# Performance work log

Hardware: AMD Instinct MI355X
Metric: run time of the kernel (lower is better)

The kernel has to match this reference:

```python
import jax, jax.numpy as jnp
import numpy as np
from jax import lax

B, T, D, U, M = 64, 800, 3, 400, 20


def _lstm_peephole(x, Wx, Wh, b, p_i, p_f, p_o):
    """Peephole LSTM over [B,T,Din] -> [B,T,U]. Gate order: i,f,c,o."""
    xW = jnp.einsum('btd,dg->btg', x, Wx) + b  # precompute input projection [B,T,4U]
    h0 = jnp.zeros((x.shape[0], U), x.dtype)
    c0 = jnp.zeros((x.shape[0], U), x.dtype)

    def step(carry, xt):
        h, c = carry
        z = xt + h @ Wh
        zi, zf, zc, zo = jnp.split(z, 4, axis=-1)
        i = jax.nn.sigmoid(zi + p_i * c)
        f = jax.nn.sigmoid(zf + p_f * c)
        c_new = f * c + i * jnp.tanh(zc)
        o = jax.nn.sigmoid(zo + p_o * c_new)
        h_new = o * jnp.tanh(c_new)
        return (h_new, c_new), h_new

    _, hs = lax.scan(step, (h0, c0), jnp.swapaxes(xW, 0, 1))  # [T,B,U]
    return jnp.swapaxes(hs, 0, 1)


def _mdn(h, Wmdn, bmdn):
    y = h @ Wmdn + bmdn  # [B,T,6M+1]
    pi = jax.nn.softmax(y[..., :M], axis=-1)
    mu1 = y[..., M:2 * M]
    mu2 = y[..., 2 * M:3 * M]
    s1 = jnp.exp(y[..., 3 * M:4 * M])
    s2 = jnp.exp(y[..., 4 * M:5 * M])
    rho = jnp.tanh(y[..., 5 * M:6 * M])
    eos = jax.nn.sigmoid(y[..., 6 * M:])
    return jnp.concatenate([pi, mu1, mu2, s1, s2, rho, eos], axis=-1)


def setup_inputs() -> dict:
    key = jax.random.key(0)
    ks = jax.random.split(key, 32)
    s = 0.08
    inp = {'x': jax.random.normal(ks[0], (B, T, D), jnp.float32)}
    k = 1
    for l in range(3):
        din = D if l == 0 else D + U
        inp[f'Wx{l}'] = jax.random.normal(ks[k], (din, 4 * U), jnp.float32) * s; k += 1
        inp[f'Wh{l}'] = jax.random.normal(ks[k], (U, 4 * U), jnp.float32) * s; k += 1
        inp[f'b{l}'] = jnp.zeros((4 * U,), jnp.float32)
        inp[f'peep_i{l}'] = jax.random.normal(ks[k], (U,), jnp.float32) * s; k += 1
        inp[f'peep_f{l}'] = jax.random.normal(ks[k], (U,), jnp.float32) * s; k += 1
        inp[f'peep_o{l}'] = jax.random.normal(ks[k], (U,), jnp.float32) * s; k += 1
    inp['Wmdn'] = jax.random.normal(ks[k], (U, 6 * M + 1), jnp.float32) * s
    inp['bmdn'] = jnp.zeros((6 * M + 1,), jnp.float32)
    return inp


def reference(x, Wx0, Wh0, b0, peep_i0, peep_f0, peep_o0,
              Wx1, Wh1, b1, peep_i1, peep_f1, peep_o1,
              Wx2, Wh2, b2, peep_i2, peep_f2, peep_o2,
              Wmdn, bmdn):
    h = _lstm_peephole(x, Wx0, Wh0, b0, peep_i0, peep_f0, peep_o0)
    # skip connections: layers 1,2 take concat([inputs, prev_hidden])
    h = _lstm_peephole(jnp.concatenate([x, h], axis=-1), Wx1, Wh1, b1, peep_i1, peep_f1, peep_o1)
    h = _lstm_peephole(jnp.concatenate([x, h], axis=-1), Wx2, Wh2, b2, peep_i2, peep_f2, peep_o2)
    return _mdn(h, Wmdn, bmdn)
```

## Files before the change

kernel.cpp:

```cpp
#include <hip/hip_runtime.h>


#define TSTEPS 800
#define NG 4
#define GB 16
#define NSL 5
#define UB 80
#define CB 320
#define KP 416
#define RD 16
#define HXD 4
#define AS 424
#define ZS 332

typedef __attribute__((ext_vector_type(8))) __bf16 bf16x8;
typedef __attribute__((ext_vector_type(4))) float floatx4;

struct Peeps { const float* pi[3]; const float* pf[3]; const float* po[3]; };

__device__ __forceinline__ unsigned short f2bf(float f) {
    unsigned int u = __float_as_uint(f);
    return (unsigned short)((u + 0x7FFFu + ((u >> 16) & 1u)) >> 16);
}
__device__ __forceinline__ float bf_lo(unsigned u) { return __uint_as_float(u << 16); }
__device__ __forceinline__ float bf_hi(unsigned u) { return __uint_as_float(u & 0xFFFF0000u); }
__device__ __forceinline__ float sigm_(float v) { return 1.f / (1.f + __expf(-v)); }
__device__ __forceinline__ float tanh_(float v) { float e = __expf(2.f * v); return 1.f - 2.f / (e + 1.f); }
__device__ __forceinline__ unsigned ld_a(const unsigned* p) {
    return __hip_atomic_load(p, __ATOMIC_RELAXED, __HIP_MEMORY_SCOPE_AGENT);
}
__device__ __forceinline__ void st_a(unsigned* p, unsigned v) {
    __hip_atomic_store(p, v, __ATOMIC_RELAXED, __HIP_MEMORY_SCOPE_AGENT);
}

__global__ void pack_rec(const float* __restrict__ Wx, const float* __restrict__ Wh,
                         const float* __restrict__ bias, unsigned short* __restrict__ dst,
                         int is_l0) {
    int idx = blockIdx.x * 256 + threadIdx.x;
    if (idx >= 1600 * KP) return;
    int col = idx / KP, k = idx - col * KP;
    int co = (col & 3) * 400 + (col >> 2);
    float v = 0.f;
    if (k < 400) v = Wh[k * 1600 + co];
    else if (is_l0) {
        if (k < 403) v = Wx[(k - 400) * 1600 + co];
        else if (k == 403) v = bias[co];
    }
    dst[idx] = f2bf(v);
}
__global__ void pack_pre(const float* __restrict__ Wx, const float* __restrict__ bias,
                         unsigned short* __restrict__ dst) {
    int idx = blockIdx.x * 256 + threadIdx.x;
    if (idx >= 1600 * KP) return;
    int col = idx / KP, k = idx - col * KP;
    int co = (col & 3) * 400 + (col >> 2);
    float v = 0.f;
    if (k < 400) v = Wx[(3 + k) * 1600 + co];
    else if (k < 403) v = Wx[(k - 400) * 1600 + co];
    else if (k == 403) v = bias[co];
    dst[idx] = f2bf(v);
}
__global__ void pack_x(const float* __restrict__ x, unsigned short* __restrict__ xp) {
    int idx = blockIdx.x * 256 + threadIdx.x;
    if (idx >= TSTEPS * 64) return;
    int t = idx / 64, b = idx - t * 64;
    unsigned short o[4];
    for (int d = 0; d < 3; ++d) o[d] = f2bf(x[(b * TSTEPS + t) * 3 + d]);
    o[3] = 0x3F80u;
    *(uint2*)(xp + (size_t)idx * 4) = *(uint2*)o;
}
__global__ void pack_mdn(const float* __restrict__ Wm, const float* __restrict__ bm,
                         unsigned short* __restrict__ dst) {
    int idx = blockIdx.x * 256 + threadIdx.x;
    if (idx >= 128 * KP) return;
    int col = idx / KP, k = idx - col * KP;
    float v = 0.f;
    if (col < 121) {
        if (k < 400) v = Wm[k * 121 + col];
        else if (k == 400) v = bm[col];
    }
    dst[idx] = f2bf(v);
}

__global__ __launch_bounds__(640)
void fused_scan(const unsigned short* __restrict__ Bp,
                const unsigned short* __restrict__ Bpre,
                const unsigned short* __restrict__ xpack,
                unsigned* __restrict__ hx,
                unsigned* __restrict__ hring,
                unsigned* __restrict__ zin,
                unsigned* __restrict__ seqb,
                unsigned* __restrict__ h2,
                Peeps pp) {
    const int tid = threadIdx.x;
    const int lane = tid & 63;
    const int w = tid >> 6;
    const int bid = blockIdx.x;

    const int xcd = bid & 7;
    const int slot = bid >> 3;
    int g, rl = -1, rs = 0, plz = -1, psp = 0;
    if (xcd < 4) {
        g = xcd;
        if (slot < 5)       { rl = 0; rs = slot; }
        else if (slot < 10) { rl = 2; rs = slot - 5; }
        else                { plz = 1; psp = slot - 10; }
    } else {
        g = xcd - 4;
        if (slot < 5)       { rl = 1; rs = slot; }
        else if (slot < 10) { plz = 0; psp = slot - 5; }
        else return;
    }

    __shared__ unsigned short A[32 * AS];
    __shared__ float Z[16 * ZS];

    for (int i = tid; i < 32 * AS; i += 640) A[i] = 0;

    const int er = tid / 40;
    const int up = tid - er * 40;
    const int aoff = (lane & 15) * AS + ((lane >> 4) << 3);
    const int zc0 = w * 32 + (lane & 15);
    const int zr = (lane >> 4) << 2;

    if (rl >= 0) {
        const int l = rl;
        const int s = rs;
        bf16x8 breg[2][13];
        #pragma unroll
        for (int n = 0; n < 2; ++n) {
            const unsigned short* bpp = Bp + (size_t)l * 1600 * KP
                + (size_t)(s * CB + w * 32 + n * 16 + (lane & 15)) * KP + ((lane >> 4) << 3);
            #pragma unroll
            for (int kt = 0; kt < 13; ++kt) breg[n][kt] = *(const bf16x8*)(bpp + kt * 32);
        }
        unsigned* hxL = hx + (size_t)(l * NG + g) * HXD * 6400;
        unsigned* ringL = hring + (size_t)(l * NG + g) * RD * 3200;
        const unsigned* zinL = zin + (size_t)((l - 1) * NG + g) * RD * 12800;
        unsigned* FHown = seqb + ((l * NG + g) * NSL + s) * 16;
        const unsigned* FZup = seqb + (60 + ((l - 1) * NG + g) * NSL) * 16;
        const unsigned* FZdn = seqb + (60 + (l * NG + g) * NSL) * 16;

        const int p0 = ((s + 1) % 5) * 80, p1 = ((s + 2) % 5) * 80;
        const int p2 = ((s + 3) % 5) * 80, p3 = ((s + 4) % 5) * 80;
        const int ug0 = s * UB + 2 * up;
        const float pi0 = pp.pi[l][ug0], pi1 = pp.pi[l][ug0 + 1];
        const float pf0 = pp.pf[l][ug0], pf1 = pp.pf[l][ug0 + 1];
        const float po0 = pp.po[l][ug0], po1 = pp.po[l][ug0 + 1];
        float c0 = 0.f, c1 = 0.f;

        __syncthreads();
        if (l == 0 && tid < 16)
            *(uint2*)(&A[tid * AS + 400]) = *(const uint2*)(xpack + ((size_t)0 * 64 + g * 16 + tid) * 4);
        __syncthreads();

        for (int t = 0; t < TSTEPS; ++t) {
            {
                const unsigned want = (unsigned)(t - 1) << 16;
                const unsigned* hb = hxL + (size_t)((t + 3) & 3) * 6400 + er * 400 + 2 * up;
                const unsigned* fp = nullptr; unsigned fneed = 0;
                if (l > 0 && (t & 3) == 0 && tid < NSL) { fp = FZup + tid * 16; fneed = (unsigned)(t + 4); }
                else if (l < 2 && (t & 7) == 0 && tid >= NSL && tid < 2 * NSL) {
                    fp = FZdn + (tid - NSL) * 16; fneed = (unsigned)(t > 8 ? t - 8 : 0);
                }
                unsigned v0, v1, v2, v3, v4, v5, v6, v7;
                for (;;) {
                    bool ok = true;
                    if (t > 0) {
                        v0 = ld_a(hb + p0); v1 = ld_a(hb + p0 + 1);
                        v2 = ld_a(hb + p1); v3 = ld_a(hb + p1 + 1);
                        v4 = ld_a(hb + p2); v5 = ld_a(hb + p2 + 1);
                        v6 = ld_a(hb + p3); v7 = ld_a(hb + p3 + 1);
                        ok = ((v0 & 0xFFFF0000u) == want) & ((v1 & 0xFFFF0000u) == want) &
                             ((v2 & 0xFFFF0000u) == want) & ((v3 & 0xFFFF0000u) == want) &
                             ((v4 & 0xFFFF0000u) == want) & ((v5 & 0xFFFF0000u) == want) &
                             ((v6 & 0xFFFF0000u) == want) & ((v7 & 0xFFFF0000u) == want);
                    }
                    if (fp) ok &= (ld_a(fp) >= fneed);
                    if (__all(ok)) break;
                }
                if (t > 0) {
                    const int ab = er * AS + 2 * up;
                    *(unsigned*)&A[ab + p0] = (v0 & 0xFFFFu) | (v1 << 16);
                    *(unsigned*)&A[ab + p1] = (v2 & 0xFFFFu) | (v3 << 16);
                    *(unsigned*)&A[ab + p2] = (v4 & 0xFFFFu) | (v5 << 16);
                    *(unsigned*)&A[ab + p3] = (v6 & 0xFFFFu) | (v7 << 16);
                }
            }
            __syncthreads();
            if (tid == 0) st_a(FHown, (unsigned)t);

            unsigned q0, q1, q2, q3;
            if (l > 0) {
                const unsigned* zp = zinL + (size_t)(t & 15) * 12800 + er * 800 + 4 * (s * 40 + up);
                q0 = ld_a(zp); q1 = ld_a(zp + 1); q2 = ld_a(zp + 2); q3 = ld_a(zp + 3);
            }

            floatx4 a0 = {0, 0, 0, 0}, a1 = {0, 0, 0, 0};
            #pragma unroll
            for (int kt = 0; kt < 13; ++kt) {
                bf16x8 a = *(const bf16x8*)(&A[aoff + kt * 32]);
                a0 = __builtin_amdgcn_mfma_f32_16x16x32_bf16(a, breg[0][kt], a0, 0, 0, 0);
                a1 = __builtin_amdgcn_mfma_f32_16x16x32_bf16(a, breg[1][kt], a1, 0, 0, 0);
            }
            #pragma unroll
            for (int ri = 0; ri < 4; ++ri) {
                Z[(zr + ri) * ZS + zc0] = a0[ri];
                Z[(zr + ri) * ZS + zc0 + 16] = a1[ri];
            }
            __syncthreads();

            float4 za = *(const float4*)(&Z[er * ZS + 8 * up]);
            float4 zb4 = *(const float4*)(&Z[er * ZS + 8 * up + 4]);
            if (l > 0) {
                za.x += bf_lo(q0); za.y += bf_hi(q0); za.z += bf_lo(q1); za.w += bf_hi(q1);
                zb4.x += bf_lo(q2); zb4.y += bf_hi(q2); zb4.z += bf_lo(q3); zb4.w += bf_hi(q3);
            }
            float iv = sigm_(za.x + pi0 * c0);
            float fv = sigm_(za.y + pf0 * c0);
            float cn = fv * c0 + iv * tanh_(za.z);
            float ov = sigm_(za.w + po0 * cn);
            float h0 = ov * tanh_(cn);
            c0 = cn;
            iv = sigm_(zb4.x + pi1 * c1);
            fv = sigm_(zb4.y + pf1 * c1);
            cn = fv * c1 + iv * tanh_(zb4.z);
            ov = sigm_(zb4.w + po1 * cn);
            float h1 = ov * tanh_(cn);
            c1 = cn;
            unsigned packh = (unsigned)f2bf(h0) | ((unsigned)f2bf(h1) << 16);
            *(unsigned*)&A[er * AS + ug0] = packh;
            if (l == 0 && tid < 16 && t + 1 < TSTEPS)
                *(uint2*)(&A[tid * AS + 400]) = *(const uint2*)(xpack + ((size_t)(t + 1) * 64 + g * 16 + tid) * 4);
            __syncthreads();

            unsigned* hxs = hxL + (size_t)(t & 3) * 6400 + er * 400 + ug0;
            st_a(hxs, ((unsigned)t << 16) | (packh & 0xFFFFu));
            st_a(hxs + 1, ((unsigned)t << 16) | (packh >> 16));
            if (l < 2)
                st_a(ringL + (size_t)(t & 15) * 3200 + er * 200 + s * 40 + up, packh);
            else
                h2[(size_t)t * 12800 + (g * GB + er) * 200 + s * 40 + up] = packh;
        }
        __syncthreads();
        if (tid == 0) st_a(FHown, (unsigned)TSTEPS);
    } else {
        const int lz = plz;
        const int sp = psp;
        bf16x8 breg[2][13];
        #pragma unroll
        for (int n = 0; n < 2; ++n) {
            const unsigned short* bpp = Bpre + (size_t)lz * 1600 * KP
                + (size_t)(sp * CB + w * 32 + n * 16 + (lane & 15)) * KP + ((lane >> 4) << 3);
            #pragma unroll
            for (int kt = 0; kt < 13; ++kt) breg[n][kt] = *(const bf16x8*)(bpp + kt * 32);
        }
        const unsigned* ringS = hring + (size_t)(lz * NG + g) * RD * 3200;
        unsigned* zinD = zin + (size_t)(lz * NG + g) * RD * 12800;
        const unsigned* FHup = seqb + ((lz * NG + g) * NSL) * 16;
        const unsigned* FHdn = seqb + (((lz + 1) * NG + g) * NSL) * 16;
        unsigned* FZown = seqb + (60 + (lz * NG + g) * NSL + sp) * 16;
        __syncthreads();

        for (int c = 0; c < TSTEPS; c += 2) {
            {
                const unsigned* fp = nullptr; unsigned need = 0;
                if (tid < NSL) { fp = FHup + tid * 16; need = (unsigned)(c + 2); }
                else if (tid < 2 * NSL) { fp = FHdn + (tid - NSL) * 16; need = (unsigned)(c > 14 ? c - 14 : 0); }
                bool ok = (fp == nullptr) || (ld_a(fp) >= need);
                while (!__all(ok)) { if (!ok) ok = ld_a(fp) >= need; }
            }
            __syncthreads();
            if (tid == 0 && c > 0) st_a(FZown, (unsigned)c);

            for (int i = tid; i < 6400; i += 640) {
                int tc = (i >= 3200) ? 1 : 0;
                int j = i - tc * 3200;
                unsigned v = ld_a(ringS + (size_t)((c + tc) & 15) * 3200 + j);
                int r = j / 200, d = j - r * 200;
                *(unsigned*)&A[(tc * 16 + r) * AS + 2 * d] = v;
            }
            if (tid < 32) {
                int tc = tid >> 4, r = tid & 15;
                *(uint2*)(&A[(tc * 16 + r) * AS + 400]) =
                    *(const uint2*)(xpack + ((size_t)(c + tc) * 64 + g * 16 + r) * 4);
            }
            __syncthreads();

            floatx4 a00 = {0,0,0,0}, a01 = {0,0,0,0}, a10 = {0,0,0,0}, a11 = {0,0,0,0};
            #pragma unroll
            for (int kt = 0; kt < 13; ++kt) {
                bf16x8 x0 = *(const bf16x8*)(&A[aoff + kt * 32]);
                bf16x8 x1 = *(const bf16x8*)(&A[aoff + 16 * AS + kt * 32]);
                a00 = __builtin_amdgcn_mfma_f32_16x16x32_bf16(x0, breg[0][kt], a00, 0, 0, 0);
                a01 = __builtin_amdgcn_mfma_f32_16x16x32_bf16(x0, breg[1][kt], a01, 0, 0, 0);
                a10 = __builtin_amdgcn_mfma_f32_16x16x32_bf16(x1, breg[0][kt], a10, 0, 0, 0);
                a11 = __builtin_amdgcn_mfma_f32_16x16x32_bf16(x1, breg[1][kt], a11, 0, 0, 0);
            }
            #pragma unroll
            for (int m = 0; m < 2; ++m) {
                #pragma unroll
                for (int ri = 0; ri < 4; ++ri) {
                    Z[(zr + ri) * ZS + zc0] = (m ? a10[ri] : a00[ri]);
                    Z[(zr + ri) * ZS + zc0 + 16] = (m ? a11[ri] : a01[ri]);
                }
                __syncthreads();
                float4 za = *(const float4*)(&Z[er * ZS + 8 * up]);
                float4 zbv = *(const float4*)(&Z[er * ZS + 8 * up + 4]);
                unsigned* zg = zinD + (size_t)((c + m) & 15) * 12800 + er * 800 + sp * 160 + 4 * up;
                st_a(zg,     (unsigned)f2bf(za.x) | ((unsigned)f2bf(za.y) << 16));
                st_a(zg + 1, (unsigned)f2bf(za.z) | ((unsigned)f2bf(za.w) << 16));
                st_a(zg + 2, (unsigned)f2bf(zbv.x) | ((unsigned)f2bf(zbv.y) << 16));
                st_a(zg + 3, (unsigned)f2bf(zbv.z) | ((unsigned)f2bf(zbv.w) << 16));
                __syncthreads();
            }
        }
        __syncthreads();
        if (tid == 0) st_a(FZown, (unsigned)TSTEPS);
    }
}

__global__ __launch_bounds__(256)
void mdn_kernel(const unsigned short* __restrict__ h2,
                const unsigned short* __restrict__ Bm,
                float* __restrict__ out) {
    const int blk = blockIdx.x;
    const int b = blk / 25;
    const int t0 = (blk - b * 25) * 32;
    const int tid = threadIdx.x;
    const int lane = tid & 63;
    const int w = tid >> 6;
    const int m = w & 1, nh = w >> 1;

    __shared__ unsigned short A[32 * 424];
    __shared__ float Z[32 * 132];
    __shared__ float rmax[32], rinv[32];

    for (int i = tid; i < 32 * 424; i += 256) A[i] = 0;
    __syncthreads();
    for (int c = tid; c < 32 * 50; c += 256) {
        int r = c / 50, j = c - r * 50;
        *(bf16x8*)(&A[r * 424 + j * 8]) = *(const bf16x8*)(h2 + (size_t)(t0 + r) * 25600 + b * 400 + j * 8);
    }
    if (tid < 32) A[tid * 424 + 400] = 0x3F80u;
    __syncthreads();

    floatx4 acc[4] = {{0,0,0,0},{0,0,0,0},{0,0,0,0},{0,0,0,0}};
    const int aoff = (m * 16 + (lane & 15)) * 424 + ((lane >> 4) << 3);
    #pragma unroll
    for (int kt = 0; kt < 13; ++kt) {
        bf16x8 a = *(const bf16x8*)(&A[aoff + kt * 32]);
        #pragma unroll
        for (int n = 0; n < 4; ++n) {
            const unsigned short* bp = Bm + (size_t)((nh * 4 + n) * 16 + (lane & 15)) * KP
                                          + ((lane >> 4) << 3) + kt * 32;
            acc[n] = __builtin_amdgcn_mfma_f32_16x16x32_bf16(a, *(const bf16x8*)bp, acc[n], 0, 0, 0);
        }
    }
    #pragma unroll
    for (int n = 0; n < 4; ++n) {
        int zc = (nh * 4 + n) * 16 + (lane & 15);
        int zrow = m * 16 + ((lane >> 4) << 2);
        #pragma unroll
        for (int ri = 0; ri < 4; ++ri)
            Z[(zrow + ri) * 132 + zc] = acc[n][ri];
    }
    __syncthreads();
    if (tid < 32) {
        float mx = -1e30f;
        for (int j = 0; j < 20; ++j) mx = fmaxf(mx, Z[tid * 132 + j]);
        float sm = 0.f;
        for (int j = 0; j < 20; ++j) sm += __expf(Z[tid * 132 + j] - mx);
        rmax[tid] = mx;
        rinv[tid] = 1.f / sm;
    }
    __syncthreads();
    for (int idxo = tid; idxo < 32 * 121; idxo += 256) {
        int r = idxo / 121, jo = idxo - r * 121;
        float v = Z[r * 132 + jo];
        float o;
        if (jo < 20) o = __expf(v - rmax[r]) * rinv[r];
        else if (jo < 60) o = v;
        else if (jo < 100) o = __expf(v);
        else if (jo < 120) o = tanh_(v);
        else o = sigm_(v);
        out[(size_t)(b * TSTEPS + t0 + r) * 121 + jo] = o;
    }
}

extern "C" void kernel_launch(void* const* d_in, const int* in_sizes, int n_in,
                              void* d_out, int out_size, void* d_ws, size_t ws_size,
                              hipStream_t stream) {
    const float* x = (const float*)d_in[0];
    const float* Wx[3] = {(const float*)d_in[1], (const float*)d_in[7], (const float*)d_in[13]};
    const float* Wh[3] = {(const float*)d_in[2], (const float*)d_in[8], (const float*)d_in[14]};
    const float* bb[3] = {(const float*)d_in[3], (const float*)d_in[9], (const float*)d_in[15]};
    Peeps pp;
    for (int l = 0; l < 3; ++l) {
        pp.pi[l] = (const float*)d_in[4 + 6 * l];
        pp.pf[l] = (const float*)d_in[5 + 6 * l];
        pp.po[l] = (const float*)d_in[6 + 6 * l];
    }
    const float* Wm = (const float*)d_in[19];
    const float* bm = (const float*)d_in[20];
    float* out = (float*)d_out;

    char* base = (char*)d_ws;
    size_t off = 0;
    auto alloc = [&](size_t bytes) -> void* {
        void* r = base + off;
        off = (off + bytes + 255) & ~(size_t)255;
        return r;
    };
    unsigned* seqb        = (unsigned*)alloc(1600 * sizeof(unsigned));
    unsigned* hx          = (unsigned*)alloc((size_t)3 * NG * HXD * 6400 * 4);
    unsigned* hring       = (unsigned*)alloc((size_t)3 * NG * RD * 3200 * 4);
    unsigned* zin         = (unsigned*)alloc((size_t)2 * NG * RD * 12800 * 4);
    unsigned short* Bp    = (unsigned short*)alloc((size_t)3 * 1600 * KP * 2);
    unsigned short* Bpre  = (unsigned short*)alloc((size_t)2 * 1600 * KP * 2);
    unsigned short* Bm    = (unsigned short*)alloc((size_t)128 * KP * 2);
    unsigned short* xpk   = (unsigned short*)alloc((size_t)TSTEPS * 64 * 4 * 2);
    unsigned short* h2    = (unsigned short*)alloc((size_t)TSTEPS * 64 * 400 * 2);

    hipMemsetAsync(seqb, 0, 1600 * sizeof(unsigned), stream);
    hipMemsetAsync(hx, 0xAA, (size_t)3 * NG * HXD * 6400 * 4, stream);

    for (int l = 0; l < 3; ++l)
        pack_rec<<<2600, 256, 0, stream>>>(Wx[l], Wh[l], bb[l], Bp + (size_t)l * 1600 * KP, l == 0);
    pack_pre<<<2600, 256, 0, stream>>>(Wx[1], bb[1], Bpre);
    pack_pre<<<2600, 256, 0, stream>>>(Wx[2], bb[2], Bpre + (size_t)1600 * KP);
    pack_x<<<200, 256, 0, stream>>>(x, xpk);
    pack_mdn<<<208, 256, 0, stream>>>(Wm, bm, Bm);

    fused_scan<<<120, 640, 0, stream>>>(Bp, Bpre, xpk, hx, hring, zin, seqb,
                                        (unsigned*)h2, pp);

    mdn_kernel<<<1600, 256, 0, stream>>>(h2, Bm, out);
}
```

Before: 3.038 ms.

## Remap Z staging layout to avoid bank conflicts and drop barriers

Changes the LDS staging layout of MFMA gate results so each MFMA lane writes into a strided slot. The elementwise threads then read their 8 gate values with stride-40 scalar loads instead of float4 loads, aiming to cut LDS bank conflicts. The recurrent loop drops the barrier after the h write. The precompute path double-buffers Z so both timesteps are staged and read under one barrier instead of four. Removing barriers relies on later synchronisation to protect the A and Z buffers; if any hazard remains, the results can race.

```diff
diff --git a/kernel.cpp b/kernel.cpp
--- a/kernel.cpp
+++ b/kernel.cpp
@@ -113,15 +113,16 @@
     }
 
     __shared__ unsigned short A[32 * AS];
-    __shared__ float Z[16 * ZS];
+    __shared__ float Z[2 * 16 * ZS];
 
     for (int i = tid; i < 32 * AS; i += 640) A[i] = 0;
 
     const int er = tid / 40;
     const int up = tid - er * 40;
-    const int aoff = (lane & 15) * AS + ((lane >> 4) << 3);
-    const int zc0 = w * 32 + (lane & 15);
+    const int cc = lane & 15;
+    const int aoff = cc * AS + ((lane >> 4) << 3);
     const int zr = (lane >> 4) << 2;
+    const int slotA = (cc & 7) * 40 + w * 4 + (cc >> 3);
 
     if (rl >= 0) {
         const int l = rl;
@@ -130,7 +131,7 @@
         #pragma unroll
         for (int n = 0; n < 2; ++n) {
             const unsigned short* bpp = Bp + (size_t)l * 1600 * KP
-                + (size_t)(s * CB + w * 32 + n * 16 + (lane & 15)) * KP + ((lane >> 4) << 3);
+                + (size_t)(s * CB + w * 32 + n * 16 + cc) * KP + ((lane >> 4) << 3);
             #pragma unroll
             for (int kt = 0; kt < 13; ++kt) breg[n][kt] = *(const bf16x8*)(bpp + kt * 32);
         }
@@ -205,13 +206,17 @@
             }
             #pragma unroll
             for (int ri = 0; ri < 4; ++ri) {
-                Z[(zr + ri) * ZS + zc0] = a0[ri];
-                Z[(zr + ri) * ZS + zc0 + 16] = a1[ri];
+                Z[(zr + ri) * ZS + slotA] = a0[ri];
+                Z[(zr + ri) * ZS + slotA + 2] = a1[ri];
             }
             __syncthreads();
 
-            float4 za = *(const float4*)(&Z[er * ZS + 8 * up]);
-            float4 zb4 = *(const float4*)(&Z[er * ZS + 8 * up + 4]);
+            float zv[8];
+            #pragma unroll
+            for (int k = 0; k < 8; ++k)
+                zv[k] = Z[er * ZS + 40 * k + up];
+            float4 za = {zv[0], zv[1], zv[2], zv[3]};
+            float4 zb4 = {zv[4], zv[5], zv[6], zv[7]};
             if (l > 0) {
                 za.x += bf_lo(q0); za.y += bf_hi(q0); za.z += bf_lo(q1); za.w += bf_hi(q1);
                 zb4.x += bf_lo(q2); zb4.y += bf_hi(q2); zb4.z += bf_lo(q3); zb4.w += bf_hi(q3);
@@ -232,7 +237,6 @@
             *(unsigned*)&A[er * AS + ug0] = packh;
             if (l == 0 && tid < 16 && t + 1 < TSTEPS)
                 *(uint2*)(&A[tid * AS + 400]) = *(const uint2*)(xpack + ((size_t)(t + 1) * 64 + g * 16 + tid) * 4);
-            __syncthreads();
 
             unsigned* hxs = hxL + (size_t)(t & 3) * 6400 + er * 400 + ug0;
             st_a(hxs, ((unsigned)t << 16) | (packh & 0xFFFFu));
@@ -251,7 +255,7 @@
         #pragma unroll
         for (int n = 0; n < 2; ++n) {
             const unsigned short* bpp = Bpre + (size_t)lz * 1600 * KP
-                + (size_t)(sp * CB + w * 32 + n * 16 + (lane & 15)) * KP + ((lane >> 4) << 3);
+                + (size_t)(sp * CB + w * 32 + n * 16 + cc) * KP + ((lane >> 4) << 3);
             #pragma unroll
             for (int kt = 0; kt < 13; ++kt) breg[n][kt] = *(const bf16x8*)(bpp + kt * 32);
         }
@@ -298,22 +302,30 @@
                 a11 = __builtin_amdgcn_mfma_f32_16x16x32_bf16(x1, breg[1][kt], a11, 0, 0, 0);
             }
             #pragma unroll
-            for (int m = 0; m < 2; ++m) {
-                #pragma unroll
-                for (int ri = 0; ri < 4; ++ri) {
-                    Z[(zr + ri) * ZS + zc0] = (m ? a10[ri] : a00[ri]);
-                    Z[(zr + ri) * ZS + zc0 + 16] = (m ? a11[ri] : a01[ri]);
-                }
-                __syncthreads();
-                float4 za = *(const float4*)(&Z[er * ZS + 8 * up]);
-                float4 zbv = *(const float4*)(&Z[er * ZS + 8 * up + 4]);
-                unsigned* zg = zinD + (size_t)((c + m) & 15) * 12800 + er * 800 + sp * 160 + 4 * up;
-                st_a(zg,     (unsigned)f2bf(za.x) | ((unsigned)f2bf(za.y) << 16));
-                st_a(zg + 1, (unsigned)f2bf(za.z) | ((unsigned)f2bf(za.w) << 16));
-                st_a(zg + 2, (unsigned)f2bf(zbv.x) | ((unsigned)f2bf(zbv.y) << 16));
-                st_a(zg + 3, (unsigned)f2bf(zbv.z) | ((unsigned)f2bf(zbv.w) << 16));
-                __syncthreads();
-            }
+            for (int ri = 0; ri < 4; ++ri) {
+                Z[(zr + ri) * ZS + slotA] = a00[ri];
+                Z[(zr + ri) * ZS + slotA + 2] = a01[ri];
+                Z[16 * ZS + (zr + ri) * ZS + slotA] = a10[ri];
+                Z[16 * ZS + (zr + ri) * ZS + slotA + 2] = a11[ri];
+            }
+            __syncthreads();
+
+            float zv0[8], zv1[8];
+            #pragma unroll
+            for (int k = 0; k < 8; ++k) {
+                zv0[k] = Z[er * ZS + 40 * k + up];
+                zv1[k] = Z[16 * ZS + er * ZS + 40 * k + up];
+            }
+            unsigned* zg0 = zinD + (size_t)(c & 15) * 12800 + er * 800 + sp * 160 + 4 * up;
+            unsigned* zg1 = zinD + (size_t)((c + 1) & 15) * 12800 + er * 800 + sp * 160 + 4 * up;
+            st_a(zg0,     (unsigned)f2bf(zv0[0]) | ((unsigned)f2bf(zv0[1]) << 16));
+            st_a(zg0 + 1, (unsigned)f2bf(zv0[2]) | ((unsigned)f2bf(zv0[3]) << 16));
+            st_a(zg0 + 2, (unsigned)f2bf(zv0[4]) | ((unsigned)f2bf(zv0[5]) << 16));
+            st_a(zg0 + 3, (unsigned)f2bf(zv0[6]) | ((unsigned)f2bf(zv0[7]) << 16));
+            st_a(zg1,     (unsigned)f2bf(zv1[0]) | ((unsigned)f2bf(zv1[1]) << 16));
+            st_a(zg1 + 1, (unsigned)f2bf(zv1[2]) | ((unsigned)f2bf(zv1[3]) << 16));
+            st_a(zg1 + 2, (unsigned)f2bf(zv1[4]) | ((unsigned)f2bf(zv1[5]) << 16));
+            st_a(zg1 + 3, (unsigned)f2bf(zv1[6]) | ((unsigned)f2bf(zv1[7]) << 16));
         }
         __syncthreads();
         if (tid == 0) st_a(FZown, (unsigned)TSTEPS);
```

After: 3.690 ms. +21.5%, slower.

## Split input-projection workers into even/odd timestep-pair groups for more parallel blocks

Applied to the files above, without the earlier changes.

Doubles the number of precompute (input projection) blocks per layer, with each group handling alternating 2-step chunks (stride 4) under its own progress flag. Recurrent blocks now wait on both even and odd flag sets before consuming projected inputs. The grid grows from 120 to 160 blocks and the flag buffer is enlarged. The aim is to keep the projection producers ahead of the recurrent consumers so that fewer timesteps stall on them, at the cost of more blocks that spin-wait and more flag polling.

```diff
diff --git a/kernel.cpp b/kernel.cpp
--- a/kernel.cpp
+++ b/kernel.cpp
@@ -99,16 +99,18 @@
 
     const int xcd = bid & 7;
     const int slot = bid >> 3;
-    int g, rl = -1, rs = 0, plz = -1, psp = 0;
+    int g, rl = -1, rs = 0, plz = -1, psp = 0, par = 0;
     if (xcd < 4) {
         g = xcd;
         if (slot < 5)       { rl = 0; rs = slot; }
         else if (slot < 10) { rl = 2; rs = slot - 5; }
-        else                { plz = 1; psp = slot - 10; }
+        else if (slot < 15) { plz = 1; psp = slot - 10; par = 0; }
+        else                { plz = 1; psp = slot - 15; par = 1; }
     } else {
         g = xcd - 4;
         if (slot < 5)       { rl = 1; rs = slot; }
-        else if (slot < 10) { plz = 0; psp = slot - 5; }
+        else if (slot < 10) { plz = 0; psp = slot - 5; par = 0; }
+        else if (slot < 15) { plz = 0; psp = slot - 10; par = 1; }
         else return;
     }
 
@@ -138,8 +140,10 @@
         unsigned* ringL = hring + (size_t)(l * NG + g) * RD * 3200;
         const unsigned* zinL = zin + (size_t)((l - 1) * NG + g) * RD * 12800;
         unsigned* FHown = seqb + ((l * NG + g) * NSL + s) * 16;
-        const unsigned* FZup = seqb + (60 + ((l - 1) * NG + g) * NSL) * 16;
-        const unsigned* FZdn = seqb + (60 + (l * NG + g) * NSL) * 16;
+        const unsigned* FZupE = seqb + (60 + ((0 + (l - 1)) * NG + g) * NSL) * 16;
+        const unsigned* FZupO = seqb + (60 + ((2 + (l - 1)) * NG + g) * NSL) * 16;
+        const unsigned* FZdnE = seqb + (60 + ((0 + l) * NG + g) * NSL) * 16;
+        const unsigned* FZdnO = seqb + (60 + ((2 + l) * NG + g) * NSL) * 16;
 
         const int p0 = ((s + 1) % 5) * 80, p1 = ((s + 2) % 5) * 80;
         const int p2 = ((s + 3) % 5) * 80, p3 = ((s + 4) % 5) * 80;
@@ -159,9 +163,13 @@
                 const unsigned want = (unsigned)(t - 1) << 16;
                 const unsigned* hb = hxL + (size_t)((t + 3) & 3) * 6400 + er * 400 + 2 * up;
                 const unsigned* fp = nullptr; unsigned fneed = 0;
-                if (l > 0 && (t & 3) == 0 && tid < NSL) { fp = FZup + tid * 16; fneed = (unsigned)(t + 4); }
-                else if (l < 2 && (t & 7) == 0 && tid >= NSL && tid < 2 * NSL) {
-                    fp = FZdn + (tid - NSL) * 16; fneed = (unsigned)(t > 8 ? t - 8 : 0);
+                if (l > 0 && (t & 3) == 0 && tid < 2 * NSL) {
+                    fp = (tid < NSL) ? (FZupE + tid * 16) : (FZupO + (tid - NSL) * 16);
+                    fneed = (unsigned)(t + 4);
+                } else if (l < 2 && (t & 7) == 0 && tid >= 2 * NSL && tid < 4 * NSL) {
+                    fp = (tid < 3 * NSL) ? (FZdnE + (tid - 2 * NSL) * 16)
+                                         : (FZdnO + (tid - 3 * NSL) * 16);
+                    fneed = (unsigned)(t > 8 ? t - 8 : 0);
                 }
                 unsigned v0, v1, v2, v3, v4, v5, v6, v7;
                 for (;;) {
@@ -259,10 +267,11 @@
         unsigned* zinD = zin + (size_t)(lz * NG + g) * RD * 12800;
         const unsigned* FHup = seqb + ((lz * NG + g) * NSL) * 16;
         const unsigned* FHdn = seqb + (((lz + 1) * NG + g) * NSL) * 16;
-        unsigned* FZown = seqb + (60 + (lz * NG + g) * NSL + sp) * 16;
+        unsigned* FZown = seqb + (60 + ((par * 2 + lz) * NG + g) * NSL + sp) * 16;
+        const int cstart = par * 2;
         __syncthreads();
 
-        for (int c = 0; c < TSTEPS; c += 2) {
+        for (int c = cstart; c < TSTEPS; c += 4) {
             {
                 const unsigned* fp = nullptr; unsigned need = 0;
                 if (tid < NSL) { fp = FHup + tid * 16; need = (unsigned)(c + 2); }
@@ -271,7 +280,7 @@
                 while (!__all(ok)) { if (!ok) ok = ld_a(fp) >= need; }
             }
             __syncthreads();
-            if (tid == 0 && c > 0) st_a(FZown, (unsigned)c);
+            if (tid == 0 && c > cstart) st_a(FZown, (unsigned)c);
 
             for (int i = tid; i < 6400; i += 640) {
                 int tc = (i >= 3200) ? 1 : 0;
@@ -412,7 +421,7 @@
         off = (off + bytes + 255) & ~(size_t)255;
         return r;
     };
-    unsigned* seqb        = (unsigned*)alloc(1600 * sizeof(unsigned));
+    unsigned* seqb        = (unsigned*)alloc(4096 * sizeof(unsigned));
     unsigned* hx          = (unsigned*)alloc((size_t)3 * NG * HXD * 6400 * 4);
     unsigned* hring       = (unsigned*)alloc((size_t)3 * NG * RD * 3200 * 4);
     unsigned* zin         = (unsigned*)alloc((size_t)2 * NG * RD * 12800 * 4);
@@ -422,7 +431,7 @@
     unsigned short* xpk   = (unsigned short*)alloc((size_t)TSTEPS * 64 * 4 * 2);
     unsigned short* h2    = (unsigned short*)alloc((size_t)TSTEPS * 64 * 400 * 2);
 
-    hipMemsetAsync(seqb, 0, 1600 * sizeof(unsigned), stream);
+    hipMemsetAsync(seqb, 0, 4096 * sizeof(unsigned), stream);
     hipMemsetAsync(hx, 0xAA, (size_t)3 * NG * HXD * 6400 * 4, stream);
 
     for (int l = 0; l < 3; ++l)
@@ -432,7 +441,7 @@
     pack_x<<<200, 256, 0, stream>>>(x, xpk);
     pack_mdn<<<208, 256, 0, stream>>>(Wm, bm, Bm);
 
-    fused_scan<<<120, 640, 0, stream>>>(Bp, Bpre, xpk, hx, hring, zin, seqb,
+    fused_scan<<<160, 640, 0, stream>>>(Bp, Bpre, xpk, hx, hring, zin, seqb,
                                         (unsigned*)h2, pp);
 
     mdn_kernel<<<1600, 256, 0, stream>>>(h2, Bm, out);
```

New measurement: 3.243 ms. 1.07x slower.
